# Kernel optimization log

Measured on AMD Instinct MI355X. Metric: run time of the kernel, lower is better.

Reference implementation:

```python
import jax, jax.numpy as jnp
import numpy as np

B, S, H, E, D = 4, 4096, 1024, 8, 256

def setup_inputs() -> dict:
    key = jax.random.key(0)
    k0, k1, k2, k3, k4 = jax.random.split(key, 5)
    scale_h = 1.0 / np.sqrt(H)
    scale_d = 1.0 / np.sqrt(D)
    return {
        "x": jax.random.normal(k0, (B, S, H), dtype=jnp.float32),
        "gate_w": jax.random.normal(k1, (E, H), dtype=jnp.float32) * scale_h,  # nn.Linear(H,E) weight [E,H]
        "wg": jax.random.normal(k2, (E, H, D), dtype=jnp.float32) * scale_h,   # gate_proj per expert
        "wu": jax.random.normal(k3, (E, H, D), dtype=jnp.float32) * scale_h,   # up_proj per expert
        "wd": jax.random.normal(k4, (E, D, H), dtype=jnp.float32) * scale_d,   # down_proj per expert
    }

def reference(x, gate_w, wg, wu, wd):
    b, s, h = x.shape
    xf = x.reshape(-1, h)                                   # [T, H]
    logits = jnp.einsum('th,eh->te', xf, gate_w)            # router logits
    expert_idx = jnp.argmax(logits, axis=-1)                # top-1 expert per token
    onehot = jax.nn.one_hot(expert_idx, gate_w.shape[0], dtype=x.dtype)  # [T, E]
    g = jnp.einsum('th,ehd->etd', xf, wg)                   # [E, T, D]
    u = jnp.einsum('th,ehd->etd', xf, wu)                   # [E, T, D]
    inter = jnp.square(jax.nn.relu(g)) * u                  # ReLU^2 * up
    inter = inter * onehot.T[:, :, None]                    # zero out non-selected (expert, token) pairs
    out = jnp.einsum('etd,edh->th', inter, wd)              # combine over experts
    return out.reshape(b, s, h)
```

## Files before the change

kernel.cpp:

```cpp
#include <hip/hip_runtime.h>
#include <hip/hip_bf16.h>

#define TOK 16384
#define HD  1024
#define DD  256
#define NE  8

typedef __attribute__((ext_vector_type(8))) short short8;
typedef __attribute__((ext_vector_type(4))) float floatx4;
typedef unsigned short u16;

static __device__ __forceinline__ u16 f2bf(float f) {
  __hip_bfloat16 h = __float2bfloat16(f);
  return *reinterpret_cast<u16*>(&h);
}
static __device__ __forceinline__ short8 cvt8(const float* p) {
  float4 a = *(const float4*)p;
  float4 b = *(const float4*)(p + 4);
  u16 t[8] = {f2bf(a.x), f2bf(a.y), f2bf(a.z), f2bf(a.w),
              f2bf(b.x), f2bf(b.y), f2bf(b.z), f2bf(b.w)};
  return *(short8*)t;
}

__global__ __launch_bounds__(256) void prep_kernel(
    const float* __restrict__ wg, const float* __restrict__ wu,
    const float* __restrict__ wd, const float* __restrict__ x,
    const float* __restrict__ gw,
    u16* __restrict__ wgT, u16* __restrict__ wuT, u16* __restrict__ wdT,
    int* __restrict__ counts, int* __restrict__ tlist)
{
  __shared__ u16 tile[64][72];
  __shared__ int sexp[64];
  __shared__ int sbase[NE];
  int bid = blockIdx.x;
  int tid = threadIdx.x;

  if (bid < 1536) {
    const float* src; u16* dst; int R, C;
    if (bid < 512)       { src = wg; dst = wgT; R = HD; C = DD; }
    else if (bid < 1024) { src = wu; dst = wuT; R = HD; C = DD; bid -= 512; }
    else                 { src = wd; dst = wdT; R = DD; C = HD; bid -= 1024; }
    int e = bid >> 6, t = bid & 63;
    int ntc = C >> 6;
    int tr = t / ntc, tc = t % ntc;
    int r = tid >> 2, c0 = (tid & 3) * 16;
    const float* s = src + (size_t)e * R * C + (size_t)(tr * 64 + r) * C + tc * 64 + c0;
    *(short8*)&tile[r][c0]     = cvt8(s);
    *(short8*)&tile[r][c0 + 8] = cvt8(s + 8);
    __syncthreads();
    int c = tid >> 2, r0 = (tid & 3) * 16;
    alignas(16) u16 buf[16];
    for (int j = 0; j < 16; ++j) buf[j] = tile[r0 + j][c];
    u16* d = dst + (size_t)e * R * C + (size_t)(tc * 64 + c) * R + tr * 64 + r0;
    *(float4*)(d)     = *(const float4*)&buf[0];
    *(float4*)(d + 8) = *(const float4*)&buf[8];
    return;
  }

  int lane = tid & 63, wave = tid >> 6;
  int tok0 = (bid - 1536) * 64;
  for (int i = 0; i < 16; ++i) {
    int t = tok0 + wave * 16 + i;
    const float* xp = x + (size_t)t * HD + lane * 16;
    float4 x0 = *(const float4*)xp,       x1 = *(const float4*)(xp + 4);
    float4 x2 = *(const float4*)(xp + 8), x3 = *(const float4*)(xp + 12);
    float acc[NE];
    for (int e = 0; e < NE; ++e) {
      const float* gp = gw + e * HD + lane * 16;
      float4 g0 = *(const float4*)gp,       g1 = *(const float4*)(gp + 4);
      float4 g2 = *(const float4*)(gp + 8), g3 = *(const float4*)(gp + 12);
      acc[e] = x0.x*g0.x + x0.y*g0.y + x0.z*g0.z + x0.w*g0.w
             + x1.x*g1.x + x1.y*g1.y + x1.z*g1.z + x1.w*g1.w
             + x2.x*g2.x + x2.y*g2.y + x2.z*g2.z + x2.w*g2.w
             + x3.x*g3.x + x3.y*g3.y + x3.z*g3.z + x3.w*g3.w;
    }
    for (int off = 32; off >= 1; off >>= 1)
      for (int e = 0; e < NE; ++e) acc[e] += __shfl_xor(acc[e], off, 64);
    if (lane == 0) {
      int be = 0; float bv = acc[0];
      for (int e = 1; e < NE; ++e) if (acc[e] > bv) { bv = acc[e]; be = e; }
      sexp[wave * 16 + i] = be;
    }
  }
  __syncthreads();
  if (tid < NE) {
    int c = 0;
    for (int i = 0; i < 64; ++i) c += (sexp[i] == tid) ? 1 : 0;
    sbase[tid] = c ? atomicAdd(&counts[tid], c) : 0;
  }
  __syncthreads();
  if (tid < 64) {
    int e = sexp[tid], rank = 0;
    for (int i = 0; i < tid; ++i) rank += (sexp[i] == e) ? 1 : 0;
    tlist[e * TOK + sbase[e] + rank] = tok0 + tid;
  }
}

__global__ __launch_bounds__(256) void gemm1_kernel(
    const float* __restrict__ x, const u16* __restrict__ wgT,
    const u16* __restrict__ wuT,
    const int* __restrict__ counts, const int* __restrict__ tlist,
    u16* __restrict__ inter)
{
  int bid = blockIdx.x;
  int e = bid & 7, half = (bid >> 3) & 1, tile = bid >> 4;
  int cnt = counts[e];
  int row0 = tile * 64;
  if (row0 >= cnt) return;

  __shared__ int stok[64];
  __shared__ u16 xA[64][40];
  __shared__ u16 sB[256][40];

  int tid = threadIdx.x, lane = tid & 63, wave = tid >> 6;
  if (tid < 64) {
    int r = row0 + tid;
    stok[tid] = tlist[e * TOK + (r < cnt ? r : cnt - 1)];
  }
  __syncthreads();
  int rmax = cnt - row0; if (rmax > 64) rmax = 64;

  int col = lane & 15, quad = lane >> 4;
  int at = tid >> 2, ac = (tid & 3) * 8;
  const float* axp = x + (size_t)stok[at] * HD + ac;

  const u16* bp[4];
  for (int i = 0; i < 4; ++i) {
    int id = i * 256 + tid;
    int n = id >> 2, c = (id & 3) * 8;
    const u16* base = (n < 128) ? (wgT + ((size_t)e * DD + half * 128 + n) * HD)
                                : (wuT + ((size_t)e * DD + half * 128 + (n - 128)) * HD);
    bp[i] = base + c;
  }

  floatx4 acc[4][4];
  floatx4 zz = {0.f, 0.f, 0.f, 0.f};
  for (int m = 0; m < 4; ++m) for (int j = 0; j < 4; ++j) acc[m][j] = zz;

  for (int k0 = 0; k0 < HD; k0 += 32) {
    short8 av = cvt8(axp + k0);
    short8 bv[4];
    for (int i = 0; i < 4; ++i) bv[i] = *(const short8*)(bp[i] + k0);
    __syncthreads();
    *(short8*)&xA[at][ac] = av;
    for (int i = 0; i < 4; ++i) {
      int id = i * 256 + tid;
      *(short8*)&sB[id >> 2][(id & 3) * 8] = bv[i];
    }
    __syncthreads();
    short8 af[4], bfr[4];
    for (int m = 0; m < 4; ++m) af[m] = *(const short8*)&xA[m * 16 + col][quad * 8];
    bfr[0] = *(const short8*)&sB[wave * 32 + col][quad * 8];
    bfr[1] = *(const short8*)&sB[wave * 32 + 16 + col][quad * 8];
    bfr[2] = *(const short8*)&sB[128 + wave * 32 + col][quad * 8];
    bfr[3] = *(const short8*)&sB[128 + wave * 32 + 16 + col][quad * 8];
    for (int m = 0; m < 4; ++m)
      for (int j = 0; j < 4; ++j)
        acc[m][j] = __builtin_amdgcn_mfma_f32_16x16x32_bf16(af[m], bfr[j], acc[m][j], 0, 0, 0);
  }

  for (int m = 0; m < 4; ++m)
    for (int jj = 0; jj < 2; ++jj)
      for (int r = 0; r < 4; ++r) {
        int row = m * 16 + quad * 4 + r;
        if (row < rmax) {
          float g = acc[m][jj][r]; g = g > 0.f ? g : 0.f;
          float u = acc[m][jj + 2][r];
          inter[(size_t)stok[row] * DD + half * 128 + wave * 32 + jj * 16 + col] = f2bf(g * g * u);
        }
      }
}

__global__ __launch_bounds__(256) void gemm2_kernel(
    const u16* __restrict__ inter, const u16* __restrict__ wdT,
    const int* __restrict__ counts, const int* __restrict__ tlist,
    float* __restrict__ out)
{
  int bid = blockIdx.x;
  int e = bid & 7, q = (bid >> 3) & 3, tile = bid >> 5;
  int cnt = counts[e];
  int row0 = tile * 64;
  if (row0 >= cnt) return;
  int n0 = q * 256;

  __shared__ int stok[64];
  __shared__ u16 sA[64][40];
  __shared__ __align__(16) u16 sBraw[256 * 40];
  u16 (*sB)[40] = (u16(*)[40])sBraw;
  float (*st)[260] = (float(*)[260])sBraw;

  int tid = threadIdx.x, lane = tid & 63, wave = tid >> 6;
  if (tid < 64) {
    int r = row0 + tid;
    stok[tid] = tlist[e * TOK + (r < cnt ? r : cnt - 1)];
  }
  __syncthreads();
  int rmax = cnt - row0; if (rmax > 64) rmax = 64;

  int col = lane & 15, quad = lane >> 4;
  int at = tid >> 2, ac = (tid & 3) * 8;
  const u16* aip = inter + (size_t)stok[at] * DD + ac;

  floatx4 acc[4][4];
  floatx4 zz = {0.f, 0.f, 0.f, 0.f};
  for (int m = 0; m < 4; ++m) for (int j = 0; j < 4; ++j) acc[m][j] = zz;

  for (int k0 = 0; k0 < DD; k0 += 32) {
    short8 av = *(const short8*)(aip + k0);
    short8 bv[4];
    for (int i = 0; i < 4; ++i) {
      int id = i * 256 + tid;
      int n = id >> 2, c = (id & 3) * 8;
      bv[i] = *(const short8*)(wdT + ((size_t)e * HD + n0 + n) * DD + k0 + c);
    }
    __syncthreads();
    *(short8*)&sA[at][ac] = av;
    for (int i = 0; i < 4; ++i) {
      int id = i * 256 + tid;
      *(short8*)&sB[id >> 2][(id & 3) * 8] = bv[i];
    }
    __syncthreads();
    short8 af[4], bfr[4];
    for (int m = 0; m < 4; ++m) af[m] = *(const short8*)&sA[m * 16 + col][quad * 8];
    for (int j = 0; j < 4; ++j) bfr[j] = *(const short8*)&sB[wave * 64 + j * 16 + col][quad * 8];
    for (int m = 0; m < 4; ++m)
      for (int j = 0; j < 4; ++j)
        acc[m][j] = __builtin_amdgcn_mfma_f32_16x16x32_bf16(af[m], bfr[j], acc[m][j], 0, 0, 0);
  }

  for (int m = 0; m < 4; ++m) {
    __syncthreads();
    for (int j = 0; j < 4; ++j)
      for (int r = 0; r < 4; ++r)
        st[quad * 4 + r][wave * 64 + j * 16 + col] = acc[m][j][r];
    __syncthreads();
    for (int i = 0; i < 4; ++i) {
      int id = i * 256 + tid;
      int r = id >> 6, c4 = (id & 63) * 4;
      int row = m * 16 + r;
      if (row < rmax)
        *(float4*)(out + (size_t)stok[row] * HD + n0 + c4) = *(const float4*)&st[r][c4];
    }
  }
}

extern "C" void kernel_launch(void* const* d_in, const int* in_sizes, int n_in,
                              void* d_out, int out_size, void* d_ws, size_t ws_size,
                              hipStream_t stream) {
  const float* x  = (const float*)d_in[0];
  const float* gw = (const float*)d_in[1];
  const float* wg = (const float*)d_in[2];
  const float* wu = (const float*)d_in[3];
  const float* wd = (const float*)d_in[4];
  float* out = (float*)d_out;

  char* ws = (char*)d_ws;
  int* counts = (int*)ws;
  int* tlist  = (int*)(ws + 256);
  u16* wgT   = (u16*)(ws + 524544);
  u16* wuT   = wgT + (size_t)NE * DD * HD;
  u16* wdT   = wuT + (size_t)NE * DD * HD;
  u16* inter = wdT + (size_t)NE * HD * DD;

  hipMemsetAsync(counts, 0, NE * sizeof(int), stream);
  prep_kernel<<<1792, 256, 0, stream>>>(wg, wu, wd, x, gw, wgT, wuT, wdT, counts, tlist);
  gemm1_kernel<<<4096, 256, 0, stream>>>(x, wgT, wuT, counts, tlist, inter);
  gemm2_kernel<<<8192, 256, 0, stream>>>(inter, wdT, counts, tlist, out);
}
```

Baseline: 225.6 us.

## Pre-convert x to bf16 in router pass and load A fragments directly

The router kernel now also writes a bf16 copy of x, when the workspace is large enough, and handles 16 tokens per block instead of 64, giving more blocks. Both GEMMs now load A fragments straight from global memory into registers instead of staging them through shared memory, which drops one LDS store/load round per k-step. gemm1 also stages its output through LDS so it can write inter with coalesced 16-byte stores. The intent is to halve A-operand traffic and drop repeated fp32-to-bf16 conversion in gemm1. In exchange prep writes an extra 32MB and the A loads become gathered, less-coalesced per-lane reads.

```diff
diff --git a/kernel.cpp b/kernel.cpp
--- a/kernel.cpp
+++ b/kernel.cpp
@@ -27,10 +27,11 @@
     const float* __restrict__ wd, const float* __restrict__ x,
     const float* __restrict__ gw,
     u16* __restrict__ wgT, u16* __restrict__ wuT, u16* __restrict__ wdT,
-    int* __restrict__ counts, int* __restrict__ tlist)
+    int* __restrict__ counts, int* __restrict__ tlist,
+    u16* __restrict__ xb, int use_xb)
 {
   __shared__ u16 tile[64][72];
-  __shared__ int sexp[64];
+  __shared__ int sexp[16];
   __shared__ int sbase[NE];
   int bid = blockIdx.x;
   int tid = threadIdx.x;
@@ -58,9 +59,10 @@
   }
 
   int lane = tid & 63, wave = tid >> 6;
-  int tok0 = (bid - 1536) * 64;
-  for (int i = 0; i < 16; ++i) {
-    int t = tok0 + wave * 16 + i;
+  int tok0 = (bid - 1536) * 16;
+  for (int i = 0; i < 4; ++i) {
+    int ti = wave * 4 + i;
+    int t = tok0 + ti;
     const float* xp = x + (size_t)t * HD + lane * 16;
     float4 x0 = *(const float4*)xp,       x1 = *(const float4*)(xp + 4);
     float4 x2 = *(const float4*)(xp + 8), x3 = *(const float4*)(xp + 12);
@@ -79,26 +81,36 @@
     if (lane == 0) {
       int be = 0; float bv = acc[0];
       for (int e = 1; e < NE; ++e) if (acc[e] > bv) { bv = acc[e]; be = e; }
-      sexp[wave * 16 + i] = be;
+      sexp[ti] = be;
+    }
+    if (use_xb) {
+      alignas(16) u16 b[16] = {f2bf(x0.x), f2bf(x0.y), f2bf(x0.z), f2bf(x0.w),
+                               f2bf(x1.x), f2bf(x1.y), f2bf(x1.z), f2bf(x1.w),
+                               f2bf(x2.x), f2bf(x2.y), f2bf(x2.z), f2bf(x2.w),
+                               f2bf(x3.x), f2bf(x3.y), f2bf(x3.z), f2bf(x3.w)};
+      u16* op = xb + (size_t)t * HD + lane * 16;
+      *(float4*)op       = *(const float4*)&b[0];
+      *(float4*)(op + 8) = *(const float4*)&b[8];
     }
   }
   __syncthreads();
   if (tid < NE) {
     int c = 0;
-    for (int i = 0; i < 64; ++i) c += (sexp[i] == tid) ? 1 : 0;
+    for (int i = 0; i < 16; ++i) c += (sexp[i] == tid) ? 1 : 0;
     sbase[tid] = c ? atomicAdd(&counts[tid], c) : 0;
   }
   __syncthreads();
-  if (tid < 64) {
+  if (tid < 16) {
     int e = sexp[tid], rank = 0;
     for (int i = 0; i < tid; ++i) rank += (sexp[i] == e) ? 1 : 0;
     tlist[e * TOK + sbase[e] + rank] = tok0 + tid;
   }
 }
 
-__global__ __launch_bounds__(256) void gemm1_kernel(
-    const float* __restrict__ x, const u16* __restrict__ wgT,
-    const u16* __restrict__ wuT,
+template <int USE_XB>
+static __device__ __forceinline__ void gemm1_body(
+    const float* __restrict__ x, const u16* __restrict__ xb,
+    const u16* __restrict__ wgT, const u16* __restrict__ wuT,
     const int* __restrict__ counts, const int* __restrict__ tlist,
     u16* __restrict__ inter)
 {
@@ -109,8 +121,7 @@
   if (row0 >= cnt) return;
 
   __shared__ int stok[64];
-  __shared__ u16 xA[64][40];
-  __shared__ u16 sB[256][40];
+  __shared__ __align__(16) u16 sB[256][40];
 
   int tid = threadIdx.x, lane = tid & 63, wave = tid >> 6;
   if (tid < 64) {
@@ -121,8 +132,14 @@
   int rmax = cnt - row0; if (rmax > 64) rmax = 64;
 
   int col = lane & 15, quad = lane >> 4;
-  int at = tid >> 2, ac = (tid & 3) * 8;
-  const float* axp = x + (size_t)stok[at] * HD + ac;
+
+  const u16*   arow_b[4];
+  const float* arow_f[4];
+  for (int m = 0; m < 4; ++m) {
+    int t = stok[m * 16 + col];
+    if (USE_XB) arow_b[m] = xb + (size_t)t * HD + quad * 8;
+    else        arow_f[m] = x  + (size_t)t * HD + quad * 8;
+  }
 
   const u16* bp[4];
   for (int i = 0; i < 4; ++i) {
@@ -138,18 +155,18 @@
   for (int m = 0; m < 4; ++m) for (int j = 0; j < 4; ++j) acc[m][j] = zz;
 
   for (int k0 = 0; k0 < HD; k0 += 32) {
-    short8 av = cvt8(axp + k0);
+    short8 af[4];
+    for (int m = 0; m < 4; ++m)
+      af[m] = USE_XB ? *(const short8*)(arow_b[m] + k0) : cvt8(arow_f[m] + k0);
     short8 bv[4];
     for (int i = 0; i < 4; ++i) bv[i] = *(const short8*)(bp[i] + k0);
     __syncthreads();
-    *(short8*)&xA[at][ac] = av;
     for (int i = 0; i < 4; ++i) {
       int id = i * 256 + tid;
       *(short8*)&sB[id >> 2][(id & 3) * 8] = bv[i];
     }
     __syncthreads();
-    short8 af[4], bfr[4];
-    for (int m = 0; m < 4; ++m) af[m] = *(const short8*)&xA[m * 16 + col][quad * 8];
+    short8 bfr[4];
     bfr[0] = *(const short8*)&sB[wave * 32 + col][quad * 8];
     bfr[1] = *(const short8*)&sB[wave * 32 + 16 + col][quad * 8];
     bfr[2] = *(const short8*)&sB[128 + wave * 32 + col][quad * 8];
@@ -159,16 +176,33 @@
         acc[m][j] = __builtin_amdgcn_mfma_f32_16x16x32_bf16(af[m], bfr[j], acc[m][j], 0, 0, 0);
   }
 
+  __syncthreads();
+  u16 (*st)[136] = (u16(*)[136])sB;
   for (int m = 0; m < 4; ++m)
     for (int jj = 0; jj < 2; ++jj)
       for (int r = 0; r < 4; ++r) {
         int row = m * 16 + quad * 4 + r;
-        if (row < rmax) {
-          float g = acc[m][jj][r]; g = g > 0.f ? g : 0.f;
-          float u = acc[m][jj + 2][r];
-          inter[(size_t)stok[row] * DD + half * 128 + wave * 32 + jj * 16 + col] = f2bf(g * g * u);
-        }
+        float g = acc[m][jj][r]; g = g > 0.f ? g : 0.f;
+        st[row][wave * 32 + jj * 16 + col] = f2bf(g * g * acc[m][jj + 2][r]);
       }
+  __syncthreads();
+  for (int i = 0; i < 4; ++i) {
+    int id = i * 256 + tid;
+    int row = id >> 4, c = (id & 15) * 8;
+    if (row < rmax)
+      *(float4*)(inter + (size_t)stok[row] * DD + half * 128 + c) = *(const float4*)&st[row][c];
+  }
+}
+
+__global__ __launch_bounds__(256) void gemm1_xb(
+    const u16* __restrict__ xb, const u16* __restrict__ wgT, const u16* __restrict__ wuT,
+    const int* __restrict__ counts, const int* __restrict__ tlist, u16* __restrict__ inter) {
+  gemm1_body<1>(nullptr, xb, wgT, wuT, counts, tlist, inter);
+}
+__global__ __launch_bounds__(256) void gemm1_f32(
+    const float* __restrict__ x, const u16* __restrict__ wgT, const u16* __restrict__ wuT,
+    const int* __restrict__ counts, const int* __restrict__ tlist, u16* __restrict__ inter) {
+  gemm1_body<0>(x, nullptr, wgT, wuT, counts, tlist, inter);
 }
 
 __global__ __launch_bounds__(256) void gemm2_kernel(
@@ -184,7 +218,6 @@
   int n0 = q * 256;
 
   __shared__ int stok[64];
-  __shared__ u16 sA[64][40];
   __shared__ __align__(16) u16 sBraw[256 * 40];
   u16 (*sB)[40] = (u16(*)[40])sBraw;
   float (*st)[260] = (float(*)[260])sBraw;
@@ -198,15 +231,18 @@
   int rmax = cnt - row0; if (rmax > 64) rmax = 64;
 
   int col = lane & 15, quad = lane >> 4;
-  int at = tid >> 2, ac = (tid & 3) * 8;
-  const u16* aip = inter + (size_t)stok[at] * DD + ac;
+
+  const u16* arow[4];
+  for (int m = 0; m < 4; ++m)
+    arow[m] = inter + (size_t)stok[m * 16 + col] * DD + quad * 8;
 
   floatx4 acc[4][4];
   floatx4 zz = {0.f, 0.f, 0.f, 0.f};
   for (int m = 0; m < 4; ++m) for (int j = 0; j < 4; ++j) acc[m][j] = zz;
 
   for (int k0 = 0; k0 < DD; k0 += 32) {
-    short8 av = *(const short8*)(aip + k0);
+    short8 af[4];
+    for (int m = 0; m < 4; ++m) af[m] = *(const short8*)(arow[m] + k0);
     short8 bv[4];
     for (int i = 0; i < 4; ++i) {
       int id = i * 256 + tid;
@@ -214,14 +250,12 @@
       bv[i] = *(const short8*)(wdT + ((size_t)e * HD + n0 + n) * DD + k0 + c);
     }
     __syncthreads();
-    *(short8*)&sA[at][ac] = av;
     for (int i = 0; i < 4; ++i) {
       int id = i * 256 + tid;
       *(short8*)&sB[id >> 2][(id & 3) * 8] = bv[i];
     }
     __syncthreads();
-    short8 af[4], bfr[4];
-    for (int m = 0; m < 4; ++m) af[m] = *(const short8*)&sA[m * 16 + col][quad * 8];
+    short8 bfr[4];
     for (int j = 0; j < 4; ++j) bfr[j] = *(const short8*)&sB[wave * 64 + j * 16 + col][quad * 8];
     for (int m = 0; m < 4; ++m)
       for (int j = 0; j < 4; ++j)
@@ -261,9 +295,17 @@
   u16* wuT   = wgT + (size_t)NE * DD * HD;
   u16* wdT   = wuT + (size_t)NE * DD * HD;
   u16* inter = wdT + (size_t)NE * HD * DD;
+  u16* xb    = inter + (size_t)TOK * DD;
+  size_t need_xb = 524544 + (size_t)NE * DD * HD * 2 * 3
+                 + (size_t)TOK * DD * 2 + (size_t)TOK * HD * 2;
+  int use_xb = (ws_size >= need_xb) ? 1 : 0;
 
   hipMemsetAsync(counts, 0, NE * sizeof(int), stream);
-  prep_kernel<<<1792, 256, 0, stream>>>(wg, wu, wd, x, gw, wgT, wuT, wdT, counts, tlist);
-  gemm1_kernel<<<4096, 256, 0, stream>>>(x, wgT, wuT, counts, tlist, inter);
+  prep_kernel<<<2560, 256, 0, stream>>>(wg, wu, wd, x, gw, wgT, wuT, wdT,
+                                        counts, tlist, xb, use_xb);
+  if (use_xb)
+    gemm1_xb<<<4096, 256, 0, stream>>>(xb, wgT, wuT, counts, tlist, inter);
+  else
+    gemm1_f32<<<4096, 256, 0, stream>>>(x, wgT, wuT, counts, tlist, inter);
   gemm2_kernel<<<8192, 256, 0, stream>>>(inter, wdT, counts, tlist, out);
 }
```

Result: slower. 239.5 us (+6.2%).
